# Kernel optimization log

Measured on AMD Instinct MI355X. Metric: run time of the kernel, lower is better.

Reference implementation:

```python
import jax, jax.numpy as jnp
import numpy as np

B, T, D, H = 4, 3072, 1024, 16
HD = D // H

def setup_inputs() -> dict:
    key = jax.random.key(0)
    ks = jax.random.split(key, 7)
    s = 1.0 / np.sqrt(D)
    x = jax.random.normal(ks[0], (B, T, D), dtype=jnp.float32)
    Wq = jax.random.normal(ks[1], (D, D), dtype=jnp.float32) * s
    Wk = jax.random.normal(ks[2], (D, D), dtype=jnp.float32) * s
    Wv = jax.random.normal(ks[3], (D, D), dtype=jnp.float32) * s
    Wo = jax.random.normal(ks[4], (D, D), dtype=jnp.float32) * s
    bo = jnp.zeros((D,), dtype=jnp.float32)
    Wconv = jax.random.normal(ks[5], (D, D, 3), dtype=jnp.float32) * (1.0 / np.sqrt(3 * D))  # (out, in, kw)
    return {"x": x, "Wq": Wq, "Wk": Wk, "Wv": Wv, "Wo": Wo, "bo": bo, "Wconv": Wconv}

def reference(x, Wq, Wk, Wv, Wo, bo, Wconv):
    b, t, d = x.shape
    # stride-3 conv pooling of K/V stream (Conv1d(D, D, 3, stride=3, bias=False))
    kc = jax.lax.conv_general_dilated(
        x.transpose(0, 2, 1), Wconv, window_strides=(3,), padding='VALID',
        dimension_numbers=('NCH', 'OIH', 'NCH')).transpose(0, 2, 1)  # (B, T//3, D)
    k_tmp = jnp.concatenate([x[:, :1, :], kc], axis=1)  # (B, Tk, D)
    tk = k_tmp.shape[1]
    # comparison-based bias mask: masked where 3*k_idx >= q_idx + 0.001
    q_idx = jnp.arange(t, dtype=jnp.float32)
    k_idx = jnp.arange(tk, dtype=jnp.float32)
    mask = (k_idx[None, :] * 3.0 >= q_idx[:, None] + 0.001).astype(x.dtype)  # (T, Tk)
    # projections (torch Linear: y = x @ W.T)
    q = x @ Wq.T
    k = k_tmp @ Wk.T
    v = k_tmp @ Wv.T
    q = q.reshape(b, t, H, HD).transpose(0, 2, 1, 3)   # (B, H, T, HD)
    k = k.reshape(b, tk, H, HD).transpose(0, 2, 1, 3)  # (B, H, Tk, HD)
    v = v.reshape(b, tk, H, HD).transpose(0, 2, 1, 3)
    scores = jnp.einsum('bhqd,bhkd->bhqk', q, k) * (HD ** -0.5)
    scores = scores + mask * jnp.asarray(-1e9, dtype=x.dtype)
    p = jax.nn.softmax(scores, axis=-1)  # dropout is identity in eval (p=0)
    o = jnp.einsum('bhqk,bhkd->bhqd', p, v)
    o = o.transpose(0, 2, 1, 3).reshape(b, t, d)
    return o @ Wo.T + bo
```

## Files before the change

### kernel.cpp

```cpp
#include <hip/hip_runtime.h>
#include <hip/hip_bf16.h>
#include <cstdint>
#include <cstddef>

typedef __attribute__((ext_vector_type(8))) __bf16 bf16x8;
typedef __attribute__((ext_vector_type(4))) __bf16 bf16x4;
typedef __attribute__((ext_vector_type(4))) float  floatx4;

#define MFMA16x16x32(a, b, c) __builtin_amdgcn_mfma_f32_16x16x32_bf16((a), (b), (c), 0, 0, 0)

#define ATTN_SC 0.18033688011112042f

__device__ __forceinline__ void gload_lds16(const void* g, void* l) {
  __builtin_amdgcn_global_load_lds((const __attribute__((address_space(1))) void*)g,
                                   (__attribute__((address_space(3))) void*)l,
                                   16, 0, 0);
}


__global__ void prep_kernel(const float* __restrict__ x,
                            const float* __restrict__ Wq, const float* __restrict__ Wk,
                            const float* __restrict__ Wv, const float* __restrict__ Wo,
                            const float* __restrict__ Wconv,
                            __bf16* __restrict__ xb,
                            __bf16* __restrict__ wqb, __bf16* __restrict__ wkb,
                            __bf16* __restrict__ wvb, __bf16* __restrict__ wob,
                            __bf16* __restrict__ wc2, __bf16* __restrict__ ktmp) {
  const int bid = blockIdx.x, tid = threadIdx.x;
  if (bid < 4096) {
    const int which = bid >> 10;
    const float* src = (which == 0) ? Wq : (which == 1) ? Wk : (which == 2) ? Wv : Wo;
    __bf16* dst = (which == 0) ? wqb : (which == 1) ? wkb : (which == 2) ? wvb : wob;
    const int i = (bid & 1023) * 256 + tid;
    floatx4 v = *(const floatx4*)(src + (size_t)i * 4);
    bf16x4 o; o[0] = (__bf16)v[0]; o[1] = (__bf16)v[1]; o[2] = (__bf16)v[2]; o[3] = (__bf16)v[3];
    *(bf16x4*)(dst + (size_t)i * 4) = o;
  } else if (bid < 5120) {
    const int t = (bid - 4096) * 256 + tid;
    const int o = t >> 8, c = t & 255;
    const float* base = Wconv + (size_t)o * 3072 + c * 12;
    float f[12];
    *(floatx4*)(f)     = *(const floatx4*)(base);
    *(floatx4*)(f + 4) = *(const floatx4*)(base + 4);
    *(floatx4*)(f + 8) = *(const floatx4*)(base + 8);
#pragma unroll
    for (int kw = 0; kw < 3; ++kw) {
      bf16x4 q;
#pragma unroll
      for (int j = 0; j < 4; ++j) q[j] = (__bf16)f[3 * j + kw];
      *(bf16x4*)(wc2 + (size_t)o * 3072 + kw * 1024 + c * 4) = q;
    }
  } else if (bid < 5136) {
    const int i = (bid - 5120) * 256 + tid;
    const int b = i >> 10, c = i & 1023;
    ktmp[(size_t)b * 1025 * 1024 + c] = (__bf16)x[(size_t)b * 3072 * 1024 + c];
  } else {
    const int i = (bid - 5136) * 256 + tid;
    floatx4 v = *(const floatx4*)(x + (size_t)i * 4);
    bf16x4 o; o[0] = (__bf16)v[0]; o[1] = (__bf16)v[1]; o[2] = (__bf16)v[2]; o[3] = (__bf16)v[3];
    *(bf16x4*)(xb + (size_t)i * 4) = o;
  }
}

__global__ void vtrans_kernel(const __bf16* __restrict__ V, __bf16* __restrict__ Vt) {
  __shared__ __attribute__((aligned(16))) __bf16 tile[64][72];
  const int tid = threadIdx.x;
  const int bh = blockIdx.y;
  const int b = bh >> 4, h = bh & 15;
  const int t0 = blockIdx.x * 64;
  const int r = tid >> 3, s = tid & 7;
#pragma unroll
  for (int p = 0; p < 2; ++p) {
    const int t = p * 32 + r;
    bf16x8 v = *(const bf16x8*)(V + ((size_t)(b * 1025 + t0 + t)) * 1024 + h * 64 + s * 8);
    *(bf16x8*)(&tile[t][s * 8]) = v;
  }
  __syncthreads();
#pragma unroll
  for (int p = 0; p < 2; ++p) {
    const int d = p * 32 + r;
    bf16x8 o;
#pragma unroll
    for (int e = 0; e < 8; ++e) o[e] = tile[s * 8 + e][d];
    *(bf16x8*)(Vt + ((size_t)bh * 64 + d) * 1024 + t0 + s * 8) = o;
  }
}


template <int MODE>
__device__ __forceinline__ void gemm8_body(
    const __bf16* __restrict__ A, const __bf16* __restrict__ Bw, void* __restrict__ Cout,
    const float* __restrict__ bias, int N, int K, int m0, int n0,
    __bf16* As, __bf16* Bs)
{
  const int tid  = threadIdx.x;
  const int wave = tid >> 6;
  const int lane = tid & 63;
  const int g    = lane >> 4;
  const int ln   = lane & 15;
  const int wr   = (wave >> 2) * 64;
  const int wc   = (wave & 3) * 64;

  const int prow = tid >> 3;
  const int pc   = tid & 7;
  const int ca   = pc ^ (prow & 7);
  const size_t aSrc  = (size_t)(m0 + prow + ((ca >> 2) << 6)) * K + ((ca & 3) << 3);
  const size_t bSrc0 = (size_t)(n0 + prow + ((ca >> 2) << 7)) * K + ((ca & 3) << 3);
  const size_t bSrc1 = bSrc0 + (size_t)64 * K;

  int aOff[4], bOff[4];
#pragma unroll
  for (int i = 0; i < 4; ++i) {
    const int ra = wr + i * 16 + ln;
    const int pr = ra & 63;
    const int c  = ((ra >> 6) << 2) + g;
    aOff[i] = pr * 64 + ((c ^ (pr & 7)) << 3);
  }
#pragma unroll
  for (int j = 0; j < 4; ++j) {
    const int rb = wc + j * 16 + ln;
    const int pr = rb & 127;
    const int c  = ((rb >> 7) << 2) + g;
    bOff[j] = pr * 64 + ((c ^ (pr & 7)) << 3);
  }

  floatx4 acc[4][4];
#pragma unroll
  for (int i = 0; i < 4; ++i)
#pragma unroll
    for (int j = 0; j < 4; ++j) { floatx4 z = {0.f, 0.f, 0.f, 0.f}; acc[i][j] = z; }

  __bf16* const ad0 = As + (tid << 3);
  __bf16* const bd0 = Bs + (tid << 3);

  auto STAGE = [&](int t, int s) {
    const int koff = t * 32;
    gload_lds16(A  + aSrc  + koff, ad0 + s * 4096);
    gload_lds16(Bw + bSrc0 + koff, bd0 + s * 8192);
    gload_lds16(Bw + bSrc1 + koff, bd0 + s * 8192 + 4096);
  };

  bf16x8 af[4], bf[4];

#define READF(s)                                                                   \
  {                                                                                \
    const __bf16* ah_ = As + (s) * 4096;                                           \
    const __bf16* bh_ = Bs + (s) * 8192;                                           \
    _Pragma("unroll")                                                              \
    for (int i_ = 0; i_ < 4; ++i_) af[i_] = *(const bf16x8*)(ah_ + aOff[i_]);      \
    _Pragma("unroll")                                                              \
    for (int j_ = 0; j_ < 4; ++j_) bf[j_] = *(const bf16x8*)(bh_ + bOff[j_]);      \
  }

#define MFMAC()                                                                    \
  {                                                                                \
    __builtin_amdgcn_s_setprio(1);                                                 \
    _Pragma("unroll")                                                              \
    for (int i_ = 0; i_ < 4; ++i_)                                                 \
      _Pragma("unroll")                                                            \
      for (int j_ = 0; j_ < 4; ++j_)                                               \
        acc[i_][j_] = MFMA16x16x32(af[i_], bf[j_], acc[i_][j_]);                   \
    __builtin_amdgcn_s_setprio(0);                                                 \
  }

  const int HT = K >> 5;

  STAGE(0, 0);
  STAGE(1, 1);
  asm volatile("s_waitcnt vmcnt(3)" ::: "memory");
  __builtin_amdgcn_s_barrier();
  __builtin_amdgcn_sched_barrier(0);

  int sp = 0;
  for (int h = 0; h < HT; ++h) {
    const int s2 = (sp + 2 >= 3) ? sp - 1 : sp + 2;
    READF(sp);
    if (h + 2 < HT) STAGE(h + 2, s2);
    MFMAC();
    if (h + 1 < HT) {
      if (h + 2 < HT) { asm volatile("s_waitcnt vmcnt(3) lgkmcnt(0)" ::: "memory"); }
      else            { asm volatile("s_waitcnt vmcnt(0) lgkmcnt(0)" ::: "memory"); }
      __builtin_amdgcn_s_barrier();
      __builtin_amdgcn_sched_barrier(0);
    }
    sp = (sp + 1 >= 3) ? 0 : sp + 1;
  }

#undef READF
#undef MFMAC

#pragma unroll
  for (int j = 0; j < 4; ++j) {
    const int col = n0 + wc + j * 16 + ln;
    float bj = 0.f;
    if (MODE == 2) bj = bias[col];
#pragma unroll
    for (int i = 0; i < 4; ++i)
#pragma unroll
      for (int r = 0; r < 4; ++r) {
        const int row = m0 + wr + i * 16 + g * 4 + r;
        if (MODE == 2) {
          ((float*)Cout)[(size_t)row * N + col] = acc[i][j][r] + bj;
        } else if (MODE == 1) {
          const size_t orow = (size_t)(row >> 10) * 1025 + 1 + (row & 1023);
          ((__bf16*)Cout)[orow * 1024 + col] = (__bf16)acc[i][j][r];
        } else if (MODE == 4) {
          ((__bf16*)Cout)[(size_t)row * N + col] = (__bf16)(acc[i][j][r] * ATTN_SC);
        } else {
          ((__bf16*)Cout)[(size_t)row * N + col] = (__bf16)acc[i][j][r];
        }
      }
  }
}

__global__ __launch_bounds__(512, 4) void gemm_convq_kernel(
    const __bf16* __restrict__ xb, const __bf16* __restrict__ wc2,
    const __bf16* __restrict__ wqb, __bf16* __restrict__ ktmp, __bf16* __restrict__ qb)
{
  __shared__ __attribute__((aligned(16))) __bf16 As[12288];
  __shared__ __attribute__((aligned(16))) __bf16 Bs[24576];
  const int xcd = blockIdx.x & 7, s = blockIdx.x >> 3;
  if (s < 16) {
    const int id = xcd * 16 + s;
    gemm8_body<1>(xb, wc2, ktmp, nullptr, 1024, 3072, (id >> 2) * 128, (id & 3) * 256, As, Bs);
  } else {
    const int id = xcd * 48 + (s - 16);
    gemm8_body<4>(xb, wqb, qb, nullptr, 1024, 1024, (id >> 2) * 128, (id & 3) * 256, As, Bs);
  }
}

__global__ __launch_bounds__(512, 4) void gemm_kv_kernel(
    const __bf16* __restrict__ ktmp, const __bf16* __restrict__ wkb,
    const __bf16* __restrict__ wvb, __bf16* __restrict__ kb, __bf16* __restrict__ vb)
{
  __shared__ __attribute__((aligned(16))) __bf16 As[12288];
  __shared__ __attribute__((aligned(16))) __bf16 Bs[24576];
  const int id = (blockIdx.x & 7) * 33 + (blockIdx.x >> 3);
  const int p  = (id >= 132) ? 1 : 0;
  const int rest = id - p * 132;
  gemm8_body<0>(ktmp, p ? wvb : wkb, p ? vb : kb, nullptr, 1024, 1024,
                (rest >> 2) * 128, (rest & 3) * 256, As, Bs);
}

__global__ __launch_bounds__(512, 4) void gemm_o_kernel(
    const __bf16* __restrict__ ob, const __bf16* __restrict__ wob,
    float* __restrict__ out, const float* __restrict__ bo)
{
  __shared__ __attribute__((aligned(16))) __bf16 As[12288];
  __shared__ __attribute__((aligned(16))) __bf16 Bs[24576];
  const int id = (blockIdx.x & 7) * 48 + (blockIdx.x >> 3);
  gemm8_body<2>(ob, wob, out, bo, 1024, 1024, (id >> 2) * 128, (id & 3) * 256, As, Bs);
}


__global__ __launch_bounds__(256) void attn_kernel(
    const __bf16* __restrict__ Q, const __bf16* __restrict__ Kk,
    const __bf16* __restrict__ Vt, __bf16* __restrict__ O)
{
  __shared__ __attribute__((aligned(16))) __bf16 Kd[2][64 * 64];
  __shared__ __attribute__((aligned(16))) __bf16 Vd[2][64 * 64];
  __shared__ __attribute__((aligned(16))) __bf16 Ps[4][32 * 64];

  const int tid  = threadIdx.x;
  const int wave = tid >> 6;
  const int lane = tid & 63;
  const int g    = lane >> 4;
  const int ln   = lane & 15;

  const int l    = blockIdx.x;
  const int xcd  = l & 7;
  const int b    = xcd >> 1;
  const int rest = l >> 3;
  const int h    = rest & 15;
  const int qt   = ((11 - (rest >> 4)) << 1) | (xcd & 1);
  const int q0   = qt * 128 + wave * 32;

  const size_t qrow0 = (size_t)b * 3072 + q0;
  const size_t krow0 = (size_t)b * 1025;
  const size_t vtrow = ((size_t)(b * 16 + h)) * 64;
  const int hc = h * 64;
  const int sw = (ln & 7) << 3;
  __bf16* Pw = Ps[wave];

  const int srow = lane >> 3;
  const int scol = (lane & 7) * 8;

  auto stage = [&](int kt, int bb) {
    const int kb0 = kt * 64;
#pragma unroll
    for (int i = 0; i < 2; ++i) {
      const int rr = (wave * 2 + i) * 8 + srow;
      gload_lds16(Kk + (krow0 + kb0 + rr) * 1024 + hc + scol,
                  Kd[bb] + (size_t)rr * 64 + scol);
      gload_lds16(Vt + (vtrow + rr) * 1024 + kb0 + scol,
                  Vd[bb] + (size_t)rr * 64 + scol);
    }
  };

  bf16x8 qf[2][2];
#pragma unroll
  for (int i = 0; i < 2; ++i)
#pragma unroll
    for (int kc = 0; kc < 2; ++kc)
      qf[i][kc] = *(const bf16x8*)(Q + (qrow0 + i * 16 + ln) * 1024 + hc + kc * 32 + g * 8);

  floatx4 oacc[2][4];
  floatx4 oal[2];
#pragma unroll
  for (int i = 0; i < 2; ++i) {
    floatx4 z = {0.f, 0.f, 0.f, 0.f};
    oal[i] = z;
#pragma unroll
    for (int dt = 0; dt < 4; ++dt) oacc[i][dt] = z;
  }

  bf16x8 ones;
#pragma unroll
  for (int e = 0; e < 8; ++e) ones[e] = (__bf16)1.0f;

  const int nkt_blk = (((qt * 128 + 127) / 3) >> 6) + 1;
  const int nfull   = (q0 >= 189) ? ((q0 - 189) / 192 + 1) : 0;

  stage(0, 0);

  for (int kt = 0; kt < nkt_blk; ++kt) {
    const int bb = kt & 1;
    __syncthreads();
    if (kt + 1 < nkt_blk) stage(kt + 1, bb ^ 1);
    const int kb0 = kt * 64;
    const bool masked = (kt >= nfull);

    bf16x8 kf[4][2];
#pragma unroll
    for (int jk = 0; jk < 4; ++jk)
#pragma unroll
      for (int kc = 0; kc < 2; ++kc)
        kf[jk][kc] = *(const bf16x8*)(Kd[bb] + (jk * 16 + ln) * 64 + kc * 32 + g * 8);

#pragma unroll
    for (int jk = 0; jk < 4; ++jk)
#pragma unroll
      for (int i = 0; i < 2; ++i) {
        floatx4 s = {0.f, 0.f, 0.f, 0.f};
        s = MFMA16x16x32(kf[jk][0], qf[i][0], s);
        s = MFMA16x16x32(kf[jk][1], qf[i][1], s);
        float p[4];
#pragma unroll
        for (int r = 0; r < 4; ++r) {
          float e = __builtin_amdgcn_exp2f(s[r]);
          if (masked) {
            const int key = kb0 + jk * 16 + 4 * g + r;
            const int q   = q0 + i * 16 + ln;
            e = (3 * key <= q) ? e : 0.f;
          }
          p[r] = e;
        }
        bf16x4 pk;
        pk[0] = (__bf16)p[0]; pk[1] = (__bf16)p[1]; pk[2] = (__bf16)p[2]; pk[3] = (__bf16)p[3];
        *(bf16x4*)(Pw + (i * 16 + ln) * 64 + ((jk * 16 + 4 * g) ^ sw)) = pk;
      }

#pragma unroll
    for (int kc = 0; kc < 2; ++kc) {
      bf16x8 pf0 = *(const bf16x8*)(Pw + (ln) * 64      + ((kc * 32 + g * 8) ^ sw));
      bf16x8 pf1 = *(const bf16x8*)(Pw + (16 + ln) * 64 + ((kc * 32 + g * 8) ^ sw));
      oal[0] = MFMA16x16x32(ones, pf0, oal[0]);
      oal[1] = MFMA16x16x32(ones, pf1, oal[1]);
#pragma unroll
      for (int dt = 0; dt < 4; ++dt) {
        bf16x8 vf = *(const bf16x8*)(Vd[bb] + (dt * 16 + ln) * 64 + kc * 32 + g * 8);
        oacc[0][dt] = MFMA16x16x32(vf, pf0, oacc[0][dt]);
        oacc[1][dt] = MFMA16x16x32(vf, pf1, oacc[1][dt]);
      }
    }
  }

#pragma unroll
  for (int i = 0; i < 2; ++i) {
    const float inv = 1.0f / oal[i][0];
    const size_t row = qrow0 + i * 16 + ln;
#pragma unroll
    for (int dt = 0; dt < 4; ++dt) {
      bf16x4 o4;
#pragma unroll
      for (int r = 0; r < 4; ++r) o4[r] = (__bf16)(oacc[i][dt][r] * inv);
      *(bf16x4*)(O + row * 1024 + hc + dt * 16 + 4 * g) = o4;
    }
  }
}


extern "C" void kernel_launch(void* const* d_in, const int* in_sizes, int n_in,
                              void* d_out, int out_size, void* d_ws, size_t ws_size,
                              hipStream_t stream) {
  (void)in_sizes; (void)n_in; (void)out_size; (void)ws_size;
  const float* x     = (const float*)d_in[0];
  const float* Wq    = (const float*)d_in[1];
  const float* Wk    = (const float*)d_in[2];
  const float* Wv    = (const float*)d_in[3];
  const float* Wo    = (const float*)d_in[4];
  const float* bo    = (const float*)d_in[5];
  const float* Wconv = (const float*)d_in[6];

  char* ws = (char*)d_ws;
  const size_t SZ_XQ = (size_t)12288 * 1024 * 2;
  const size_t SZ_KT = (size_t)4224 * 1024 * 2;
  const size_t SZ_W  = (size_t)1024 * 1024 * 2;

  __bf16* xb   = (__bf16*)(ws);
  __bf16* qb   = (__bf16*)(ws + SZ_XQ);
  __bf16* ktmp = (__bf16*)(ws + 2 * SZ_XQ);
  __bf16* kb   = (__bf16*)(ws + 2 * SZ_XQ + SZ_KT);
  __bf16* vb   = (__bf16*)(ws + 2 * SZ_XQ + 2 * SZ_KT);
  __bf16* wqb  = (__bf16*)(ws + 2 * SZ_XQ + 3 * SZ_KT);
  __bf16* wkb  = (__bf16*)(ws + 2 * SZ_XQ + 3 * SZ_KT + SZ_W);
  __bf16* wvb  = (__bf16*)(ws + 2 * SZ_XQ + 3 * SZ_KT + 2 * SZ_W);
  __bf16* wob  = (__bf16*)(ws + 2 * SZ_XQ + 3 * SZ_KT + 3 * SZ_W);
  __bf16* wc2  = (__bf16*)(ws + 2 * SZ_XQ + 3 * SZ_KT + 4 * SZ_W);
  __bf16* vt   = xb;

  prep_kernel<<<dim3(17424), dim3(256), 0, stream>>>(x, Wq, Wk, Wv, Wo, Wconv,
                                                     xb, wqb, wkb, wvb, wob, wc2, ktmp);
  gemm_convq_kernel<<<dim3(512), dim3(512), 0, stream>>>(xb, wc2, wqb, ktmp, qb);
  gemm_kv_kernel<<<dim3(264), dim3(512), 0, stream>>>(ktmp, wkb, wvb, kb, vb);
  vtrans_kernel<<<dim3(16, 64), dim3(256), 0, stream>>>(vb, vt);
  attn_kernel<<<dim3(1536), dim3(256), 0, stream>>>(qb, kb, vt, qb);
  gemm_o_kernel<<<dim3(384), dim3(512), 0, stream>>>(qb, wob, (float*)d_out, bo);
}
```

Before: 316.3 us.

## Switch GEMM body from 8 waves to 4 waves with 128x64 per-wave tiles

The shared GEMM body now runs with 256 threads (4 waves) per 128x256 block tile instead of 512 threads (8 waves). Each wave covers all 128 rows by 64 columns, so it holds 8x4 accumulators and reuses each B fragment across 8 MFMAs. To keep the LDS staging unchanged, each thread issues twice as many async global-to-LDS loads and the waitcnt thresholds are adjusted to match. This raises arithmetic per LDS read and halves barrier participants, but doubles per-thread accumulator registers (128 VGPRs of accumulators), which lowers occupancy and leaves fewer waves to hide latency.

```diff
diff --git a/kernel.cpp b/kernel.cpp
--- a/kernel.cpp
+++ b/kernel.cpp
@@ -88,7 +88,7 @@
 
 
 template <int MODE>
-__device__ __forceinline__ void gemm8_body(
+__device__ __forceinline__ void gemm4_body(
     const __bf16* __restrict__ A, const __bf16* __restrict__ Bw, void* __restrict__ Cout,
     const float* __restrict__ bias, int N, int K, int m0, int n0,
     __bf16* As, __bf16* Bs)
@@ -98,20 +98,24 @@
   const int lane = tid & 63;
   const int g    = lane >> 4;
   const int ln   = lane & 15;
-  const int wr   = (wave >> 2) * 64;
-  const int wc   = (wave & 3) * 64;
-
-  const int prow = tid >> 3;
-  const int pc   = tid & 7;
-  const int ca   = pc ^ (prow & 7);
-  const size_t aSrc  = (size_t)(m0 + prow + ((ca >> 2) << 6)) * K + ((ca & 3) << 3);
-  const size_t bSrc0 = (size_t)(n0 + prow + ((ca >> 2) << 7)) * K + ((ca & 3) << 3);
-  const size_t bSrc1 = bSrc0 + (size_t)64 * K;
-
-  int aOff[4], bOff[4];
-#pragma unroll
-  for (int i = 0; i < 4; ++i) {
-    const int ra = wr + i * 16 + ln;
+  const int wc   = wave * 64;
+
+  size_t aSrcv[2], bSrcv[4];
+#pragma unroll
+  for (int q = 0; q < 2; ++q) {
+    const int c = tid + q * 256, pr = c >> 3, ca = (c & 7) ^ (pr & 7);
+    aSrcv[q] = (size_t)(m0 + pr + ((ca >> 2) << 6)) * K + ((ca & 3) << 3);
+  }
+#pragma unroll
+  for (int q = 0; q < 4; ++q) {
+    const int c = tid + q * 256, pr = c >> 3, ca = (c & 7) ^ (pr & 7);
+    bSrcv[q] = (size_t)(n0 + pr + ((ca >> 2) << 7)) * K + ((ca & 3) << 3);
+  }
+
+  int aOff[8], bOff[4];
+#pragma unroll
+  for (int i = 0; i < 8; ++i) {
+    const int ra = i * 16 + ln;
     const int pr = ra & 63;
     const int c  = ((ra >> 6) << 2) + g;
     aOff[i] = pr * 64 + ((c ^ (pr & 7)) << 3);
@@ -124,30 +128,32 @@
     bOff[j] = pr * 64 + ((c ^ (pr & 7)) << 3);
   }
 
-  floatx4 acc[4][4];
-#pragma unroll
-  for (int i = 0; i < 4; ++i)
+  floatx4 acc[8][4];
+#pragma unroll
+  for (int i = 0; i < 8; ++i)
 #pragma unroll
     for (int j = 0; j < 4; ++j) { floatx4 z = {0.f, 0.f, 0.f, 0.f}; acc[i][j] = z; }
-
-  __bf16* const ad0 = As + (tid << 3);
-  __bf16* const bd0 = Bs + (tid << 3);
 
   auto STAGE = [&](int t, int s) {
     const int koff = t * 32;
-    gload_lds16(A  + aSrc  + koff, ad0 + s * 4096);
-    gload_lds16(Bw + bSrc0 + koff, bd0 + s * 8192);
-    gload_lds16(Bw + bSrc1 + koff, bd0 + s * 8192 + 4096);
+    __bf16* ad = As + s * 4096 + (tid << 3);
+    __bf16* bd = Bs + s * 8192 + (tid << 3);
+    gload_lds16(A  + aSrcv[0] + koff, ad);
+    gload_lds16(A  + aSrcv[1] + koff, ad + 2048);
+    gload_lds16(Bw + bSrcv[0] + koff, bd);
+    gload_lds16(Bw + bSrcv[1] + koff, bd + 2048);
+    gload_lds16(Bw + bSrcv[2] + koff, bd + 4096);
+    gload_lds16(Bw + bSrcv[3] + koff, bd + 6144);
   };
 
-  bf16x8 af[4], bf[4];
+  bf16x8 af[8], bf[4];
 
 #define READF(s)                                                                   \
   {                                                                                \
     const __bf16* ah_ = As + (s) * 4096;                                           \
     const __bf16* bh_ = Bs + (s) * 8192;                                           \
     _Pragma("unroll")                                                              \
-    for (int i_ = 0; i_ < 4; ++i_) af[i_] = *(const bf16x8*)(ah_ + aOff[i_]);      \
+    for (int i_ = 0; i_ < 8; ++i_) af[i_] = *(const bf16x8*)(ah_ + aOff[i_]);      \
     _Pragma("unroll")                                                              \
     for (int j_ = 0; j_ < 4; ++j_) bf[j_] = *(const bf16x8*)(bh_ + bOff[j_]);      \
   }
@@ -156,7 +162,7 @@
   {                                                                                \
     __builtin_amdgcn_s_setprio(1);                                                 \
     _Pragma("unroll")                                                              \
-    for (int i_ = 0; i_ < 4; ++i_)                                                 \
+    for (int i_ = 0; i_ < 8; ++i_)                                                 \
       _Pragma("unroll")                                                            \
       for (int j_ = 0; j_ < 4; ++j_)                                               \
         acc[i_][j_] = MFMA16x16x32(af[i_], bf[j_], acc[i_][j_]);                   \
@@ -167,7 +173,7 @@
 
   STAGE(0, 0);
   STAGE(1, 1);
-  asm volatile("s_waitcnt vmcnt(3)" ::: "memory");
+  asm volatile("s_waitcnt vmcnt(6)" ::: "memory");
   __builtin_amdgcn_s_barrier();
   __builtin_amdgcn_sched_barrier(0);
 
@@ -178,7 +184,7 @@
     if (h + 2 < HT) STAGE(h + 2, s2);
     MFMAC();
     if (h + 1 < HT) {
-      if (h + 2 < HT) { asm volatile("s_waitcnt vmcnt(3) lgkmcnt(0)" ::: "memory"); }
+      if (h + 2 < HT) { asm volatile("s_waitcnt vmcnt(6) lgkmcnt(0)" ::: "memory"); }
       else            { asm volatile("s_waitcnt vmcnt(0) lgkmcnt(0)" ::: "memory"); }
       __builtin_amdgcn_s_barrier();
       __builtin_amdgcn_sched_barrier(0);
@@ -195,10 +201,10 @@
     float bj = 0.f;
     if (MODE == 2) bj = bias[col];
 #pragma unroll
-    for (int i = 0; i < 4; ++i)
+    for (int i = 0; i < 8; ++i)
 #pragma unroll
       for (int r = 0; r < 4; ++r) {
-        const int row = m0 + wr + i * 16 + g * 4 + r;
+        const int row = m0 + i * 16 + g * 4 + r;
         if (MODE == 2) {
           ((float*)Cout)[(size_t)row * N + col] = acc[i][j][r] + bj;
         } else if (MODE == 1) {
@@ -213,7 +219,7 @@
   }
 }
 
-__global__ __launch_bounds__(512, 4) void gemm_convq_kernel(
+__global__ __launch_bounds__(256, 2) void gemm_convq_kernel(
     const __bf16* __restrict__ xb, const __bf16* __restrict__ wc2,
     const __bf16* __restrict__ wqb, __bf16* __restrict__ ktmp, __bf16* __restrict__ qb)
 {
@@ -222,14 +228,14 @@
   const int xcd = blockIdx.x & 7, s = blockIdx.x >> 3;
   if (s < 16) {
     const int id = xcd * 16 + s;
-    gemm8_body<1>(xb, wc2, ktmp, nullptr, 1024, 3072, (id >> 2) * 128, (id & 3) * 256, As, Bs);
+    gemm4_body<1>(xb, wc2, ktmp, nullptr, 1024, 3072, (id >> 2) * 128, (id & 3) * 256, As, Bs);
   } else {
     const int id = xcd * 48 + (s - 16);
-    gemm8_body<4>(xb, wqb, qb, nullptr, 1024, 1024, (id >> 2) * 128, (id & 3) * 256, As, Bs);
-  }
-}
-
-__global__ __launch_bounds__(512, 4) void gemm_kv_kernel(
+    gemm4_body<4>(xb, wqb, qb, nullptr, 1024, 1024, (id >> 2) * 128, (id & 3) * 256, As, Bs);
+  }
+}
+
+__global__ __launch_bounds__(256, 2) void gemm_kv_kernel(
     const __bf16* __restrict__ ktmp, const __bf16* __restrict__ wkb,
     const __bf16* __restrict__ wvb, __bf16* __restrict__ kb, __bf16* __restrict__ vb)
 {
@@ -238,18 +244,18 @@
   const int id = (blockIdx.x & 7) * 33 + (blockIdx.x >> 3);
   const int p  = (id >= 132) ? 1 : 0;
   const int rest = id - p * 132;
-  gemm8_body<0>(ktmp, p ? wvb : wkb, p ? vb : kb, nullptr, 1024, 1024,
+  gemm4_body<0>(ktmp, p ? wvb : wkb, p ? vb : kb, nullptr, 1024, 1024,
                 (rest >> 2) * 128, (rest & 3) * 256, As, Bs);
 }
 
-__global__ __launch_bounds__(512, 4) void gemm_o_kernel(
+__global__ __launch_bounds__(256, 2) void gemm_o_kernel(
     const __bf16* __restrict__ ob, const __bf16* __restrict__ wob,
     float* __restrict__ out, const float* __restrict__ bo)
 {
   __shared__ __attribute__((aligned(16))) __bf16 As[12288];
   __shared__ __attribute__((aligned(16))) __bf16 Bs[24576];
   const int id = (blockIdx.x & 7) * 48 + (blockIdx.x >> 3);
-  gemm8_body<2>(ob, wob, out, bo, 1024, 1024, (id >> 2) * 128, (id & 3) * 256, As, Bs);
+  gemm4_body<2>(ob, wob, out, bo, 1024, 1024, (id >> 2) * 128, (id & 3) * 256, As, Bs);
 }
 
 
@@ -421,9 +427,9 @@
 
   prep_kernel<<<dim3(17424), dim3(256), 0, stream>>>(x, Wq, Wk, Wv, Wo, Wconv,
                                                      xb, wqb, wkb, wvb, wob, wc2, ktmp);
-  gemm_convq_kernel<<<dim3(512), dim3(512), 0, stream>>>(xb, wc2, wqb, ktmp, qb);
-  gemm_kv_kernel<<<dim3(264), dim3(512), 0, stream>>>(ktmp, wkb, wvb, kb, vb);
+  gemm_convq_kernel<<<dim3(512), dim3(256), 0, stream>>>(xb, wc2, wqb, ktmp, qb);
+  gemm_kv_kernel<<<dim3(264), dim3(256), 0, stream>>>(ktmp, wkb, wvb, kb, vb);
   vtrans_kernel<<<dim3(16, 64), dim3(256), 0, stream>>>(vb, vt);
   attn_kernel<<<dim3(1536), dim3(256), 0, stream>>>(qb, kb, vt, qb);
-  gemm_o_kernel<<<dim3(384), dim3(512), 0, stream>>>(qb, wob, (float*)d_out, bo);
-}
+  gemm_o_kernel<<<dim3(384), dim3(256), 0, stream>>>(qb, wob, (float*)d_out, bo);
+}
```

Result: no change. 314.4 us (-0.6%).
